# Kernel tuning notes

Hardware: AMD Instinct MI355X
Metric: run time of the kernel (lower is better)

## Reference

```python
import jax, jax.numpy as jnp
import numpy as np
import math

N = 100000      # nodes
E = 1600000     # edges
D = 128         # in_channels
C = 256         # number of dominant-set cliques
HID = 64        # mlp_hidden
RATIO = 0.8
K = int(math.ceil(RATIO * N))  # 80000 topk nodes per view


def setup_inputs() -> dict:
    key = jax.random.key(0)
    ks = jax.random.split(key, 18)
    s = 0.05
    return {
        "x": jax.random.normal(ks[0], (N, D), jnp.float32),
        "edge_index": jax.random.randint(ks[1], (2, E), 0, N, dtype=jnp.int32),
        "batch": jnp.zeros((N,), jnp.int32),
        "cluster_id": jax.random.randint(ks[2], (N,), 0, C, dtype=jnp.int32),
        # MLP scorer: Linear(D,HID) -> ReLU -> Linear(HID,1)
        "mlp_w1": jax.random.normal(ks[3], (D, HID), jnp.float32) * s,
        "mlp_b1": jnp.zeros((HID,), jnp.float32),
        "mlp_w2": jax.random.normal(ks[4], (HID, 1), jnp.float32) * s,
        "mlp_b2": jnp.zeros((1,), jnp.float32),
        # GATConv(D, 1, heads=1)
        "gat_w": jax.random.normal(ks[5], (D, 1), jnp.float32) * s,
        "gat_a_src": jax.random.normal(ks[6], (1,), jnp.float32) * s,
        "gat_a_dst": jax.random.normal(ks[7], (1,), jnp.float32) * s,
        "gat_b": jnp.zeros((1,), jnp.float32),
        # InterChannelGCN attention Linear(2D,1) split into fine/coarse halves
        "att_w_fine": jax.random.normal(ks[8], (D,), jnp.float32) * s,
        "att_w_coarse": jax.random.normal(ks[9], (D,), jnp.float32) * s,
        "att_b": jnp.zeros((1,), jnp.float32),
        # InterChannelGCN transform Linear(D,D)
        "trans_w": jax.random.normal(ks[10], (D, D), jnp.float32) * s,
        "trans_b": jnp.zeros((D,), jnp.float32),
    }


def _inter_channel_gcn(h_fine, H_coarse, R, wa, wb, ab, tw, tb):
    # attention(Linear(2D,1)) on concat(h_fine_i, H_coarse_j) == h_fine@wa + H_coarse@wb + b
    scores = h_fine @ wa[:, None] + (H_coarse @ wb)[None, :] + ab[0]   # [K, C]
    attn = jax.nn.softmax(scores * R, axis=-1)                          # mask-by-multiply, as original
    out = attn @ H_coarse + h_fine                                      # add_self=True
    return jax.nn.relu(out @ tw + tb)                                   # normalize=False


def reference(x, edge_index, batch, cluster_id,
              mlp_w1, mlp_b1, mlp_w2, mlp_b2,
              gat_w, gat_a_src, gat_a_dst, gat_b,
              att_w_fine, att_w_coarse, att_b, trans_w, trans_b):
    src, dst = edge_index[0], edge_index[1]

    # --- DominantClustering('avg'): cluster means as coarse features ---
    counts = jax.ops.segment_sum(jnp.ones((N,), jnp.float32), cluster_id, num_segments=C)
    Hcoarse = jax.ops.segment_sum(x, cluster_id, num_segments=C) / jnp.maximum(counts, 1.0)[:, None]

    # --- feature view: MLP score + topk ---
    feature_score = (jax.nn.relu(x @ mlp_w1 + mlp_b1) @ mlp_w2 + mlp_b2)[:, 0]   # [N]
    _, feat_idx = jax.lax.top_k(feature_score, K)
    feature_view3 = x[feat_idx]
    R_feat = jax.nn.one_hot(cluster_id[feat_idx], C, dtype=x.dtype)              # relationship matrix
    fuse1 = _inter_channel_gcn(feature_view3, Hcoarse, R_feat,
                               att_w_fine, att_w_coarse, att_b, trans_w, trans_b)

    # --- local view: GATConv(D,1,heads=1) score + topk ---
    h = x @ gat_w                                                                 # [N,1]
    e = jax.nn.leaky_relu(gat_a_src[0] * h[src, 0] + gat_a_dst[0] * h[dst, 0], 0.2)  # [E]
    m = jax.ops.segment_max(e, dst, num_segments=N)
    ex = jnp.exp(e - m[dst])
    den = jax.ops.segment_sum(ex, dst, num_segments=N)
    alpha = ex / jnp.maximum(den[dst], 1e-16)
    localview_score = jax.ops.segment_sum(alpha * h[src, 0], dst, num_segments=N) + gat_b[0]
    _, local_idx = jax.lax.top_k(localview_score, K)
    local_view1 = x[local_idx]
    R_local = jax.nn.one_hot(cluster_id[local_idx], C, dtype=x.dtype)
    fuse2 = _inter_channel_gcn(local_view1, Hcoarse, R_local,
                               att_w_fine, att_w_coarse, att_b, trans_w, trans_b)

    # --- union, edge filtering + remapping (padded fixed shapes) ---
    in_feat = jnp.zeros((N,), bool).at[feat_idx].set(True)
    in_local = jnp.zeros((N,), bool).at[local_idx].set(True)
    union = in_feat | in_local
    mapping = jnp.where(union, jnp.cumsum(union.astype(jnp.int32)) - 1, -1)
    m0, m1 = mapping[src], mapping[dst]
    valid = (m0 >= 0) & (m1 >= 0)
    edge_index_topk = jnp.where(valid[None, :], jnp.stack([m0, m1]), -1)          # [2,E], -1 = dropped

    # --- fused features (faithful to original's fuse1/fuse2 index swap) ---
    A = jnp.zeros((N, D), x.dtype).at[feat_idx].set(fuse2)    # fuse2 indexed by feature topk position
    B = jnp.zeros((N, D), x.dtype).at[local_idx].set(fuse1)   # fuse1 indexed by local topk position
    both = in_feat & in_local
    Fp = jnp.where(both[:, None], (A + B) * 0.5, A + B)
    Fp = jnp.where(union[:, None], Fp, 0.0)                   # [N,D], zero outside union

    new_batch = jnp.where(union, batch, -1)
    return Fp, edge_index_topk, new_batch
```

## Files before the change

### kernel.cpp

```cpp
#include <hip/hip_runtime.h>
#include <hip/hip_bf16.h>
#include <stdint.h>

#define N 100000
#define E_ 1600000
#define D 128
#define C_ 256
#define HID 64
#define KSEL 80000
#define NB 4096
#define CHUNK 1024
#define NCHUNK ((N + CHUNK - 1) / CHUNK)
#define CSEG 32
#define NBK 782
#define BCAP 2560
#define RMAX 2048

typedef __attribute__((ext_vector_type(8))) short bf16x8;
typedef __attribute__((ext_vector_type(4))) float f32x4;

__device__ __forceinline__ unsigned enc_f(float f) {
  unsigned b = __float_as_uint(f);
  return (b & 0x80000000u) ? ~b : (b | 0x80000000u);
}
__device__ __forceinline__ float dec_f(unsigned u) {
  unsigned b = (u & 0x80000000u) ? (u ^ 0x80000000u) : ~u;
  return __uint_as_float(b);
}

__device__ __forceinline__ unsigned short f2bf(float f) {
  unsigned u = __float_as_uint(f);
  unsigned r = u + 0x7FFFu + ((u >> 16) & 1u);
  return (unsigned short)(r >> 16);
}

__global__ __launch_bounds__(256) void k_hist_cluster(const int* __restrict__ cid, int* __restrict__ ccount) {
  int n = blockIdx.x * 256 + threadIdx.x;
  if (n < N) atomicAdd(&ccount[cid[n]], 1);
}

__global__ __launch_bounds__(1024) void k_scan_small(const int* __restrict__ in0, int* __restrict__ out0, int n) {
  __shared__ int sums[1024];
  const int* in = in0 + (size_t)blockIdx.x * n;
  int* out = out0 + (size_t)blockIdx.x * n;
  int t = threadIdx.x;
  int per = (n + 1023) / 1024;
  int base = t * per;
  int loc = 0;
  for (int k = 0; k < per; ++k) { int i = base + k; if (i < n) loc += in[i]; }
  sums[t] = loc; __syncthreads();
  for (int off = 1; off < 1024; off <<= 1) {
    int v = (t >= off) ? sums[t - off] : 0;
    __syncthreads();
    sums[t] += v;
    __syncthreads();
  }
  int run = (t == 0) ? 0 : sums[t - 1];
  for (int k = 0; k < per; ++k) { int i = base + k; if (i < n) { out[i] = run; run += in[i]; } }
}

__global__ __launch_bounds__(256) void k_scatter_cluster(const int* __restrict__ cid, const int* __restrict__ cstart,
                                                         int* __restrict__ ccur, int* __restrict__ cslot) {
  int n = blockIdx.x * 256 + threadIdx.x;
  if (n < N) {
    int c = cid[n];
    int p = cstart[c] + atomicAdd(&ccur[c], 1);
    cslot[p] = n;
  }
}

__global__ __launch_bounds__(128) void k_cluster_partial(const float* __restrict__ x, const int* __restrict__ cstart,
                                                         const int* __restrict__ ccount, const int* __restrict__ cslot,
                                                         float* __restrict__ Hc) {
  int c = blockIdx.x >> 5;
  int s = blockIdx.x & (CSEG - 1);
  int d = threadIdx.x;
  int st = cstart[c], cnt = ccount[c];
  int seg = (cnt + CSEG - 1) / CSEG;
  int lo = s * seg;
  int hi = min(cnt, lo + seg);
  if (lo >= hi) return;
  float acc = 0.f;
  int k = lo;
  for (; k + 2 <= hi; k += 2) {
    int n0 = cslot[st + k], n1 = cslot[st + k + 1];
    float v0 = x[(size_t)n0 * D + d];
    float v1 = x[(size_t)n1 * D + d];
    acc += v0 + v1;
  }
  if (k < hi) acc += x[(size_t)cslot[st + k] * D + d];
  atomicAdd(&Hc[(size_t)c * D + d], acc);
}

__global__ __launch_bounds__(128) void k_mean_gdot(const int* __restrict__ ccount, const float* __restrict__ wb,
                                                   float* __restrict__ Hc, float* __restrict__ gdot) {
  __shared__ float red[128];
  int c = blockIdx.x, d = threadIdx.x;
  float hv = Hc[(size_t)c * D + d] / (float)max(ccount[c], 1);
  Hc[(size_t)c * D + d] = hv;
  red[d] = hv * wb[d];
  __syncthreads();
  if (d < 64) {
    float v = red[d] + red[d + 64];
    for (int off = 32; off; off >>= 1) v += __shfl_down(v, off);
    if (d == 0) gdot[c] = v;
  }
}

__global__ __launch_bounds__(128) void k_S_SW_HW(const float* __restrict__ Hc, const float* __restrict__ tw,
                                                 float* __restrict__ SW, float* __restrict__ HW) {
  __shared__ float Sl[128];
  int b = blockIdx.x, t = threadIdx.x;
  if (b == 0) {
    float s = 0.f;
    for (int c = 0; c < C_; ++c) s += Hc[(size_t)c * D + t];
    Sl[t] = s;
    __syncthreads();
    float acc = 0.f;
    for (int d = 0; d < D; ++d) acc = fmaf(Sl[d], tw[(size_t)d * D + t], acc);
    SW[t] = acc;
  } else {
    const float* src = Hc + (size_t)(b - 1) * D;
    float acc = 0.f;
    for (int d = 0; d < D; ++d) acc = fmaf(src[d], tw[(size_t)d * D + t], acc);
    HW[(size_t)(b - 1) * D + t] = acc;
  }
}

__global__ __launch_bounds__(128) void k_twT(const float* __restrict__ tw, unsigned short* __restrict__ twT) {
  int k = blockIdx.x;
  int o = threadIdx.x;
  twT[(size_t)o * D + k] = f2bf(tw[(size_t)k * D + o]);
}

__global__ __launch_bounds__(256, 4) void k_score64(const float* __restrict__ x, const float* __restrict__ w1,
                                                    const float* __restrict__ b1, const float* __restrict__ w2,
                                                    const float* __restrict__ b2, const float* __restrict__ gw,
                                                    const float* __restrict__ wa, float* __restrict__ scoreF,
                                                    float* __restrict__ hg, float* __restrict__ aDot,
                                                    unsigned* __restrict__ mm) {
  __shared__ float xld[64 * D];
  __shared__ unsigned bmm[2];
  int tid = threadIdx.x;
  int base = blockIdx.x * 64;
  if (tid == 0) { bmm[0] = 0u; bmm[1] = 0xFFFFFFFFu; }
#pragma unroll
  for (int k = 0; k < 8; ++k) {
    int i = k * 256 + tid;
    int r = i >> 5, cc = i & 31;
    int n = base + r;
    float4 v = make_float4(0.f, 0.f, 0.f, 0.f);
    if (n < N) v = ((const float4*)(x + (size_t)n * D))[cc];
    ((float4*)xld)[r * 32 + (cc ^ (r & 7))] = v;
  }
  __syncthreads();

  int rg = tid >> 4;
  int cg = tid & 15;
  int r0 = rg * 4;
  int c4 = cg * 4;
  float acc[4][4] = {};
  float4 wc0 = *(const float4*)(w1 + (size_t)0 * HID + c4);
  float4 wc1 = *(const float4*)(w1 + (size_t)1 * HID + c4);
  float4 wc2 = *(const float4*)(w1 + (size_t)2 * HID + c4);
  float4 wc3 = *(const float4*)(w1 + (size_t)3 * HID + c4);
  float4 xc[4];
#pragma unroll
  for (int rr = 0; rr < 4; ++rr) {
    int row = r0 + rr;
    xc[rr] = ((const float4*)xld)[row * 32 + (row & 7)];
  }
  for (int d4 = 0; d4 < D; d4 += 4) {
    float4 wn0, wn1, wn2, wn3, xn[4];
    if (d4 + 4 < D) {
      wn0 = *(const float4*)(w1 + (size_t)(d4 + 4) * HID + c4);
      wn1 = *(const float4*)(w1 + (size_t)(d4 + 5) * HID + c4);
      wn2 = *(const float4*)(w1 + (size_t)(d4 + 6) * HID + c4);
      wn3 = *(const float4*)(w1 + (size_t)(d4 + 7) * HID + c4);
      int jn = (d4 >> 2) + 1;
#pragma unroll
      for (int rr = 0; rr < 4; ++rr) {
        int row = r0 + rr;
        xn[rr] = ((const float4*)xld)[row * 32 + (jn ^ (row & 7))];
      }
    } else {
      wn0 = wn1 = wn2 = wn3 = make_float4(0.f, 0.f, 0.f, 0.f);
#pragma unroll
      for (int rr = 0; rr < 4; ++rr) xn[rr] = make_float4(0.f, 0.f, 0.f, 0.f);
    }
#pragma unroll
    for (int rr = 0; rr < 4; ++rr) {
      float4 xv = xc[rr];
      acc[rr][0] = fmaf(xv.x, wc0.x, acc[rr][0]);
      acc[rr][1] = fmaf(xv.x, wc0.y, acc[rr][1]);
      acc[rr][2] = fmaf(xv.x, wc0.z, acc[rr][2]);
      acc[rr][3] = fmaf(xv.x, wc0.w, acc[rr][3]);
      acc[rr][0] = fmaf(xv.y, wc1.x, acc[rr][0]);
      acc[rr][1] = fmaf(xv.y, wc1.y, acc[rr][1]);
      acc[rr][2] = fmaf(xv.y, wc1.z, acc[rr][2]);
      acc[rr][3] = fmaf(xv.y, wc1.w, acc[rr][3]);
      acc[rr][0] = fmaf(xv.z, wc2.x, acc[rr][0]);
      acc[rr][1] = fmaf(xv.z, wc2.y, acc[rr][1]);
      acc[rr][2] = fmaf(xv.z, wc2.z, acc[rr][2]);
      acc[rr][3] = fmaf(xv.z, wc2.w, acc[rr][3]);
      acc[rr][0] = fmaf(xv.w, wc3.x, acc[rr][0]);
      acc[rr][1] = fmaf(xv.w, wc3.y, acc[rr][1]);
      acc[rr][2] = fmaf(xv.w, wc3.z, acc[rr][2]);
      acc[rr][3] = fmaf(xv.w, wc3.w, acc[rr][3]);
    }
    wc0 = wn0; wc1 = wn1; wc2 = wn2; wc3 = wn3;
#pragma unroll
    for (int rr = 0; rr < 4; ++rr) xc[rr] = xn[rr];
  }

  float4 b1v = *(const float4*)(b1 + c4);
  float4 w2v = *(const float4*)(w2 + c4);
  float bb = b2[0];
  unsigned vmx = 0u, vmn = 0xFFFFFFFFu;
#pragma unroll
  for (int rr = 0; rr < 4; ++rr) {
    float p = fmaxf(acc[rr][0] + b1v.x, 0.f) * w2v.x
            + fmaxf(acc[rr][1] + b1v.y, 0.f) * w2v.y
            + fmaxf(acc[rr][2] + b1v.z, 0.f) * w2v.z
            + fmaxf(acc[rr][3] + b1v.w, 0.f) * w2v.w;
#pragma unroll
    for (int off = 8; off; off >>= 1) p += __shfl_xor(p, off);
    if (cg == 0) {
      int n = base + r0 + rr;
      if (n < N) {
        float sf = p + bb;
        scoreF[n] = sf;
        unsigned e = enc_f(sf);
        vmx = max(vmx, e);
        vmn = min(vmn, e);
      }
    }
  }
#pragma unroll
  for (int off = 32; off; off >>= 1) {
    vmx = max(vmx, (unsigned)__shfl_xor((int)vmx, off));
    vmn = min(vmn, (unsigned)__shfl_xor((int)vmn, off));
  }
  if ((tid & 63) == 0) { atomicMax(&bmm[0], vmx); atomicMin(&bmm[1], vmn); }

  float4 gwa = *(const float4*)(gw + c4);
  float4 gwb = *(const float4*)(gw + 64 + c4);
  float4 waa = *(const float4*)(wa + c4);
  float4 wab = *(const float4*)(wa + 64 + c4);
#pragma unroll
  for (int rr = 0; rr < 4; ++rr) {
    int row = r0 + rr;
    float4 xa = ((const float4*)xld)[row * 32 + (cg ^ (row & 7))];
    float4 xb = ((const float4*)xld)[row * 32 + ((cg + 16) ^ (row & 7))];
    float hp = xa.x * gwa.x + xa.y * gwa.y + xa.z * gwa.z + xa.w * gwa.w
             + xb.x * gwb.x + xb.y * gwb.y + xb.z * gwb.z + xb.w * gwb.w;
    float ap = xa.x * waa.x + xa.y * waa.y + xa.z * waa.z + xa.w * waa.w
             + xb.x * wab.x + xb.y * wab.y + xb.z * wab.z + xb.w * wab.w;
#pragma unroll
    for (int off = 8; off; off >>= 1) {
      hp += __shfl_xor(hp, off);
      ap += __shfl_xor(ap, off);
    }
    if (cg == 0) {
      int n = base + row;
      if (n < N) { hg[n] = hp; aDot[n] = ap; }
    }
  }
  __syncthreads();
  if (tid == 0) { atomicMax(&mm[0], bmm[0]); atomicMin(&mm[2], bmm[1]); }
}

__global__ __launch_bounds__(1024) void k_escatter(const int* __restrict__ ei, const float* __restrict__ hg,
                                                   const float* __restrict__ asrc, const float* __restrict__ adst,
                                                   int* __restrict__ gcnt, uint2* __restrict__ payload) {
  __shared__ int lcnt[NBK];
  __shared__ int lbase[NBK];
  int tid = threadIdx.x;
  for (int i = tid; i < NBK; i += 1024) lcnt[i] = 0;
  int e0 = blockIdx.x * 8192;
  int es[8], ed[8];
#pragma unroll
  for (int k = 0; k < 8; ++k) {
    int e = e0 + k * 1024 + tid;
    bool v = (e < E_);
    es[k] = v ? ei[e] : -1;
    ed[k] = v ? ei[E_ + e] : -1;
  }
  __syncthreads();
#pragma unroll
  for (int k = 0; k < 8; ++k)
    if (ed[k] >= 0) atomicAdd(&lcnt[ed[k] >> 7], 1);
  __syncthreads();
  for (int i = tid; i < NBK; i += 1024) {
    int c = lcnt[i];
    lbase[i] = c ? atomicAdd(&gcnt[i], c) : 0;
    lcnt[i] = 0;
  }
  __syncthreads();
  float as = asrc[0], ad = adst[0];
#pragma unroll
  for (int k = 0; k < 8; ++k) {
    if (ed[k] < 0) continue;
    int s = es[k], d = ed[k];
    int b = d >> 7, dl = d & 127;
    float z = as * hg[s] + ad * hg[d];
    float ev = (z > 0.f) ? z : 0.2f * z;
    int pos = lbase[b] + atomicAdd(&lcnt[b], 1);
    if (pos < BCAP) {
      uint2 rec;
      rec.x = __float_as_uint(ev);
      rec.y = (unsigned)s | ((unsigned)dl << 24);
      payload[(size_t)b * BCAP + pos] = rec;
    }
  }
}

__global__ __launch_bounds__(256) void k_esoftmax(const uint2* __restrict__ payload, const int* __restrict__ gcnt,
                                                  const float* __restrict__ hg, const float* __restrict__ gb,
                                                  float* __restrict__ scoreL, unsigned* __restrict__ mm) {
  __shared__ unsigned mS[128];
  __shared__ float dS[128];
  __shared__ float nS[128];
  __shared__ unsigned bmm[2];
  int b = blockIdx.x;
  int tid = threadIdx.x;
  if (tid < 128) { mS[tid] = 0u; dS[tid] = 0.f; nS[tid] = 0.f; }
  if (tid == 0) { bmm[0] = 0u; bmm[1] = 0xFFFFFFFFu; }
  __syncthreads();
  int cnt = min(gcnt[b], BCAP);
  const uint2* bp = payload + (size_t)b * BCAP;
  for (int i = tid; i < cnt; i += 256) {
    uint2 r = bp[i];
    atomicMax(&mS[r.y >> 24], enc_f(__uint_as_float(r.x)));
  }
  __syncthreads();
  for (int i = tid; i < cnt; i += 256) {
    uint2 r = bp[i];
    int d = r.y >> 24;
    float ex = expf(__uint_as_float(r.x) - dec_f(mS[d]));
    float h = hg[r.y & 0xFFFFFFu];
    atomicAdd(&dS[d], ex);
    atomicAdd(&nS[d], ex * h);
  }
  __syncthreads();
  unsigned vmx = 0u, vmn = 0xFFFFFFFFu;
  if (tid < 128) {
    int dst = b * 128 + tid;
    if (dst < N) {
      float sl = nS[tid] / fmaxf(dS[tid], 1e-16f) + gb[0];
      scoreL[dst] = sl;
      unsigned e = enc_f(sl);
      vmx = e; vmn = e;
    }
  }
#pragma unroll
  for (int off = 32; off; off >>= 1) {
    vmx = max(vmx, (unsigned)__shfl_xor((int)vmx, off));
    vmn = min(vmn, (unsigned)__shfl_xor((int)vmn, off));
  }
  if ((tid & 63) == 0) { atomicMax(&bmm[0], vmx); atomicMin(&bmm[1], vmn); }
  __syncthreads();
  if (tid == 0) { atomicMax(&mm[1], bmm[0]); atomicMin(&mm[3], bmm[1]); }
}

__global__ __launch_bounds__(256) void k_bucket_hist2(const float* __restrict__ sc2, const unsigned* __restrict__ mm,
                                                      int* __restrict__ bucket2, int* __restrict__ hist2) {
  int v = blockIdx.y;
  int n = blockIdx.x * 256 + threadIdx.x;
  if (n >= N) return;
  const float* sc = sc2 + (size_t)v * N;
  float smax = dec_f(mm[v]), smin = dec_f(mm[2 + v]);
  float range = smax - smin;
  float scale = (range > 0.f) ? ((float)NB / range) : 0.f;
  float t = (smax - sc[n]) * scale;
  int b = (int)t;
  b = b < 0 ? 0 : (b > NB - 1 ? NB - 1 : b);
  bucket2[(size_t)v * N + n] = b;
  atomicAdd(&hist2[v * NB + b], 1);
}

__global__ __launch_bounds__(256) void k_bucket_scatter2(const int* __restrict__ bucket2, const int* __restrict__ start2,
                                                         int* __restrict__ cur2, int* __restrict__ slot2) {
  int v = blockIdx.y;
  int n = blockIdx.x * 256 + threadIdx.x;
  if (n >= N) return;
  int b = bucket2[(size_t)v * N + n];
  slot2[(size_t)v * N + start2[v * NB + b] + atomicAdd(&cur2[v * NB + b], 1)] = n;
}

__global__ __launch_bounds__(64) void k_bucket_rank3(const float* __restrict__ sc2, const int* __restrict__ start2,
                                                     const int* __restrict__ hist2, const int* __restrict__ slot2,
                                                     int* __restrict__ rank2, int* __restrict__ sorted2) {
  __shared__ unsigned long long keys[RMAX];
  int v = blockIdx.y;
  int b = blockIdx.x;
  int st = start2[v * NB + b], cnt = hist2[v * NB + b];
  if (cnt == 0) return;
  const float* sc = sc2 + (size_t)v * N;
  const int* slot = slot2 + (size_t)v * N;
  int* rank = rank2 + (size_t)v * N;
  int* sorted = sorted2 + (size_t)v * N;
  int tid = threadIdx.x;
  if (cnt <= RMAX) {
    for (int i = tid; i < cnt; i += 64) {
      int m = slot[st + i];
      keys[i] = (((unsigned long long)(~enc_f(sc[m]))) << 32) | (unsigned)m;
    }
    __syncthreads();
    for (int i = tid; i < cnt; i += 64) {
      unsigned long long mykey = keys[i];
      int r = 0;
      for (int j = 0; j < cnt; ++j) r += (keys[j] < mykey) ? 1 : 0;
      int m = (int)(mykey & 0xFFFFFFFFu);
      rank[m] = st + r;
      sorted[st + r] = m;
    }
  } else {
    for (int i = tid; i < cnt; i += 64) {
      int m = slot[st + i];
      unsigned long long mykey = (((unsigned long long)(~enc_f(sc[m]))) << 32) | (unsigned)m;
      int r = 0;
      for (int j = 0; j < cnt; ++j) {
        int mj = slot[st + j];
        unsigned long long k = (((unsigned long long)(~enc_f(sc[mj]))) << 32) | (unsigned)mj;
        r += (k < mykey) ? 1 : 0;
      }
      rank[m] = st + r;
      sorted[st + r] = m;
    }
  }
}

__global__ __launch_bounds__(1024) void k_union_chunksum(const int* __restrict__ rankF, const int* __restrict__ rankL,
                                                         int* __restrict__ csum) {
  __shared__ int red[1024];
  int t = threadIdx.x; int i = blockIdx.x * 1024 + t;
  int u = (i < N) ? (((rankF[i] < KSEL) || (rankL[i] < KSEL)) ? 1 : 0) : 0;
  red[t] = u; __syncthreads();
  for (int off = 512; off; off >>= 1) { if (t < off) red[t] += red[t + off]; __syncthreads(); }
  if (t == 0) csum[blockIdx.x] = red[0];
}

__global__ __launch_bounds__(1024) void k_union_map(const int* __restrict__ rankF, const int* __restrict__ rankL,
                                                    const int* __restrict__ cstart, const int* __restrict__ batch,
                                                    int* __restrict__ mapping, float* __restrict__ outBatch) {
  __shared__ int sums[1024];
  int t = threadIdx.x; int i = blockIdx.x * 1024 + t;
  int u = (i < N) ? (((rankF[i] < KSEL) || (rankL[i] < KSEL)) ? 1 : 0) : 0;
  sums[t] = u; __syncthreads();
  for (int off = 1; off < 1024; off <<= 1) {
    int v = (t >= off) ? sums[t - off] : 0;
    __syncthreads();
    sums[t] += v;
    __syncthreads();
  }
  if (i < N) {
    mapping[i] = u ? (cstart[blockIdx.x] + sums[t] - 1) : -1;
    outBatch[i] = u ? (float)batch[i] : -1.0f;
  }
}

__global__ __launch_bounds__(256) void k_edge_out(const int* __restrict__ ei, const int* __restrict__ mapping,
                                                  float* __restrict__ outE) {
  int e = blockIdx.x * 256 + threadIdx.x;
  if (e >= E_) return;
  int m0 = mapping[ei[e]], m1 = mapping[ei[E_ + e]];
  bool valid = (m0 >= 0) && (m1 >= 0);
  outE[e] = valid ? (float)m0 : -1.f;
  outE[E_ + e] = valid ? (float)m1 : -1.f;
}

__global__ __launch_bounds__(256) void k_zero_rows(const int* __restrict__ mapping, float* __restrict__ Fp) {
  int i = blockIdx.x * 256 + threadIdx.x;
  int n = i >> 5;
  if (n < N && mapping[n] < 0) ((float4*)Fp)[i] = make_float4(0.f, 0.f, 0.f, 0.f);
}

__global__ __launch_bounds__(256, 4) void k_fuse64(const float* __restrict__ x, const unsigned short* __restrict__ twT,
                                                   const float* __restrict__ tb, const float* __restrict__ SW,
                                                   const float* __restrict__ HW, const float* __restrict__ gdot,
                                                   const float* __restrict__ aDot, const int* __restrict__ cid,
                                                   const int* __restrict__ srcL, const int* __restrict__ tgtL,
                                                   const float* __restrict__ attb, const int* __restrict__ rankF,
                                                   float* __restrict__ Fp, int accum) {
  __shared__ __align__(16) unsigned xw[64 * 64];
  __shared__ float pq[64 * 2];
  __shared__ int mt[64 * 2];
  __shared__ int ft[64];
  int tid = threadIdx.x;
  int base = blockIdx.x * 64;
  if (tid < 64) {
    int ws = srcL[base + tid];
    int cc = cid[ws];
    int tg = tgtL[base + tid];
    mt[tid * 2] = cc;
    mt[tid * 2 + 1] = tg;
    ft[tid] = (rankF[tg] < KSEL) ? 1 : 0;
    float s = aDot[ws] + gdot[cc] + attb[0];
    float mx = fmaxf(s, 0.f);
    float esm = expf(s - mx), eom = expf(-mx);
    float dn = esm + 255.f * eom;
    pq[tid * 2] = esm / dn;
    pq[tid * 2 + 1] = eom / dn;
  }
#pragma unroll
  for (int k = 0; k < 8; ++k) {
    int i = k * 256 + tid;
    int r = i >> 5, c4 = i & 31;
    int ws = srcL[base + r];
    float4 v = ((const float4*)(x + (size_t)ws * D))[c4];
    uint2 pk;
    pk.x = (unsigned)f2bf(v.x) | ((unsigned)f2bf(v.y) << 16);
    pk.y = (unsigned)f2bf(v.z) | ((unsigned)f2bf(v.w) << 16);
    int u2 = r * 32 + (c4 ^ ((r & 7) << 1));
    ((uint2*)xw)[u2] = pk;
  }
  __syncthreads();

  int w = tid >> 6;
  int l = tid & 63;
  int nl = l & 15;
  int khalf = l >> 4;
  int row = w * 16 + nl;

  f32x4 acc[8] = {};
  const char* xbase = (const char*)xw + row * 256;
  unsigned rsw = (unsigned)((row & 7) << 4);
  bf16x8 bfr[4];
#pragma unroll
  for (int ks = 0; ks < 4; ++ks)
    bfr[ks] = *(const bf16x8*)(xbase + (((unsigned)(ks * 64 + khalf * 16)) ^ rsw));
#pragma unroll
  for (int ks = 0; ks < 4; ++ks) {
#pragma unroll
    for (int ot = 0; ot < 8; ++ot) {
      bf16x8 afrag = *(const bf16x8*)(twT + (size_t)(ot * 16 + nl) * D + ks * 32 + khalf * 8);
      acc[ot] = __builtin_amdgcn_mfma_f32_16x16x32_bf16(afrag, bfr[ks], acc[ot], 0, 0, 0);
    }
  }

  float p = pq[row * 2], q = pq[row * 2 + 1];
  int cc = mt[row * 2];
  int tgt = mt[row * 2 + 1];
  int doAcc = accum && ft[row];
#pragma unroll
  for (int ot = 0; ot < 8; ++ot) {
    int ch = ot * 16 + khalf * 4;
    float4 tbv = *(const float4*)(tb + ch);
    float4 swv = *(const float4*)(SW + ch);
    float4 hw = *(const float4*)(HW + (size_t)cc * D + ch);
    float4 o;
    o.x = fmaxf(acc[ot][0] + tbv.x + q * swv.x + (p - q) * hw.x, 0.f);
    o.y = fmaxf(acc[ot][1] + tbv.y + q * swv.y + (p - q) * hw.y, 0.f);
    o.z = fmaxf(acc[ot][2] + tbv.z + q * swv.z + (p - q) * hw.z, 0.f);
    o.w = fmaxf(acc[ot][3] + tbv.w + q * swv.w + (p - q) * hw.w, 0.f);
    float4* dst = (float4*)(Fp + (size_t)tgt * D + ch);
    if (doAcc) {
      float4 old = *dst;
      o.x = (o.x + old.x) * 0.5f;
      o.y = (o.y + old.y) * 0.5f;
      o.z = (o.z + old.z) * 0.5f;
      o.w = (o.w + old.w) * 0.5f;
    }
    *dst = o;
  }
}

extern "C" void kernel_launch(void* const* d_in, const int* in_sizes, int n_in,
                              void* d_out, int out_size, void* d_ws, size_t ws_size,
                              hipStream_t stream) {
  const float* x   = (const float*)d_in[0];
  const int* ei    = (const int*)d_in[1];
  const int* batch = (const int*)d_in[2];
  const int* cid   = (const int*)d_in[3];
  const float* w1  = (const float*)d_in[4];
  const float* b1  = (const float*)d_in[5];
  const float* w2  = (const float*)d_in[6];
  const float* b2  = (const float*)d_in[7];
  const float* gw  = (const float*)d_in[8];
  const float* gas = (const float*)d_in[9];
  const float* gad = (const float*)d_in[10];
  const float* gb  = (const float*)d_in[11];
  const float* wa  = (const float*)d_in[12];
  const float* wb  = (const float*)d_in[13];
  const float* ab  = (const float*)d_in[14];
  const float* tw  = (const float*)d_in[15];
  const float* tb  = (const float*)d_in[16];
  (void)in_sizes; (void)n_in; (void)ws_size; (void)out_size;

  char* p = (char*)d_ws;
  auto alloc = [&](size_t bytes) -> char* {
    char* r = p;
    p += (bytes + 255) & ~(size_t)255;
    return r;
  };
  int* ccount    = (int*)alloc(C_ * 4);
  int* ccur      = (int*)alloc(C_ * 4);
  unsigned* mm   = (unsigned*)alloc(16);
  int* hist2     = (int*)alloc(2 * NB * 4);
  int* cur2      = (int*)alloc(2 * NB * 4);
  float* Hc      = (float*)alloc((size_t)C_ * D * 4);
  int* gcnt      = (int*)alloc(NBK * 4);
  size_t zeroBytes = (size_t)(p - (char*)d_ws);
  int* cstart   = (int*)alloc(C_ * 4);
  int* cslot    = (int*)alloc((size_t)N * 4);
  float* gdot   = (float*)alloc(C_ * 4);
  float* SW     = (float*)alloc(D * 4);
  float* HW     = (float*)alloc((size_t)C_ * D * 4);
  unsigned short* twT = (unsigned short*)alloc((size_t)D * D * 2);
  float* score2 = (float*)alloc((size_t)2 * N * 4);
  float* hg     = (float*)alloc((size_t)N * 4);
  float* aDot   = (float*)alloc((size_t)N * 4);
  uint2* payload = (uint2*)alloc((size_t)NBK * BCAP * 8);
  int* bucket2  = (int*)alloc((size_t)2 * N * 4);
  int* start2   = (int*)alloc(2 * NB * 4);
  int* slot2    = (int*)alloc((size_t)2 * N * 4);
  int* sorted2  = (int*)alloc((size_t)2 * N * 4);
  int* rank2    = (int*)alloc((size_t)2 * N * 4);
  int* csums    = (int*)alloc(NCHUNK * 4);
  int* cstarts  = (int*)alloc(NCHUNK * 4);
  int* mapping  = (int*)alloc((size_t)N * 4);

  float* scoreF = score2;
  float* scoreL = score2 + N;
  int* sortedF  = sorted2;
  int* sortedL  = sorted2 + N;
  int* rankF    = rank2;
  int* rankL    = rank2 + N;

  float* outF = (float*)d_out;
  float* outE = outF + (size_t)N * D;
  float* outB = outE + (size_t)2 * E_;

  hipMemsetAsync(d_ws, 0, zeroBytes, stream);
  hipMemsetAsync(mm + 2, 0xFF, 8, stream);

  k_hist_cluster<<<(N + 255) / 256, 256, 0, stream>>>(cid, ccount);
  k_scan_small<<<1, 1024, 0, stream>>>(ccount, cstart, C_);
  k_scatter_cluster<<<(N + 255) / 256, 256, 0, stream>>>(cid, cstart, ccur, cslot);
  k_cluster_partial<<<C_ * CSEG, 128, 0, stream>>>(x, cstart, ccount, cslot, Hc);
  k_mean_gdot<<<C_, 128, 0, stream>>>(ccount, wb, Hc, gdot);
  k_S_SW_HW<<<C_ + 1, 128, 0, stream>>>(Hc, tw, SW, HW);
  k_twT<<<D, D, 0, stream>>>(tw, twT);

  k_score64<<<(N + 63) / 64, 256, 0, stream>>>(x, w1, b1, w2, b2, gw, wa, scoreF, hg, aDot, mm);
  k_escatter<<<(E_ + 8191) / 8192, 1024, 0, stream>>>(ei, hg, gas, gad, gcnt, payload);
  k_esoftmax<<<NBK, 256, 0, stream>>>(payload, gcnt, hg, gb, scoreL, mm);

  dim3 g2((N + 255) / 256, 2);
  k_bucket_hist2<<<g2, 256, 0, stream>>>(score2, mm, bucket2, hist2);
  k_scan_small<<<2, 1024, 0, stream>>>(hist2, start2, NB);
  k_bucket_scatter2<<<g2, 256, 0, stream>>>(bucket2, start2, cur2, slot2);
  dim3 gr(NB, 2);
  k_bucket_rank3<<<gr, 64, 0, stream>>>(score2, start2, hist2, slot2, rank2, sorted2);

  k_union_chunksum<<<NCHUNK, 1024, 0, stream>>>(rankF, rankL, csums);
  k_scan_small<<<1, 1024, 0, stream>>>(csums, cstarts, NCHUNK);
  k_union_map<<<NCHUNK, 1024, 0, stream>>>(rankF, rankL, cstarts, batch, mapping, outB);
  k_edge_out<<<(E_ + 255) / 256, 256, 0, stream>>>(ei, mapping, outE);
  k_zero_rows<<<(N * 32 + 255) / 256, 256, 0, stream>>>(mapping, outF);

  k_fuse64<<<KSEL / 64, 256, 0, stream>>>(x, twT, tb, SW, HW, gdot, aDot, cid, sortedL, sortedF, ab, rankF, outF, 0);
  k_fuse64<<<KSEL / 64, 256, 0, stream>>>(x, twT, tb, SW, HW, gdot, aDot, cid, sortedF, sortedL, ab, rankF, outF, 1);
}
```

Measured before the change: 566.4 us.

## Shrink edge payload to 4 bytes and recompute attention logits in softmax

The edge scatter kernel no longer computes the GAT logit or gathers hg. It writes only a packed source and local-destination word, which halves payload memory traffic. The softmax kernel caches per-bucket destination hg in shared memory and recomputes the leaky-relu logit in both passes from a gathered hg[src]. Separately, the score kernel drops the register prefetch of x tiles from LDS and the block-level min/max reduction, issuing global atomics per wavefront instead. This trades extra random hg gathers and more global atomics for less payload bandwidth and lower register pressure.

```diff
diff --git a/kernel.cpp b/kernel.cpp
--- a/kernel.cpp
+++ b/kernel.cpp
@@ -140,10 +140,8 @@
                                                     float* __restrict__ hg, float* __restrict__ aDot,
                                                     unsigned* __restrict__ mm) {
   __shared__ float xld[64 * D];
-  __shared__ unsigned bmm[2];
   int tid = threadIdx.x;
   int base = blockIdx.x * 64;
-  if (tid == 0) { bmm[0] = 0u; bmm[1] = 0xFFFFFFFFu; }
 #pragma unroll
   for (int k = 0; k < 8; ++k) {
     int i = k * 256 + tid;
@@ -164,33 +162,21 @@
   float4 wc1 = *(const float4*)(w1 + (size_t)1 * HID + c4);
   float4 wc2 = *(const float4*)(w1 + (size_t)2 * HID + c4);
   float4 wc3 = *(const float4*)(w1 + (size_t)3 * HID + c4);
-  float4 xc[4];
-#pragma unroll
-  for (int rr = 0; rr < 4; ++rr) {
-    int row = r0 + rr;
-    xc[rr] = ((const float4*)xld)[row * 32 + (row & 7)];
-  }
   for (int d4 = 0; d4 < D; d4 += 4) {
-    float4 wn0, wn1, wn2, wn3, xn[4];
+    float4 wn0, wn1, wn2, wn3;
     if (d4 + 4 < D) {
       wn0 = *(const float4*)(w1 + (size_t)(d4 + 4) * HID + c4);
       wn1 = *(const float4*)(w1 + (size_t)(d4 + 5) * HID + c4);
       wn2 = *(const float4*)(w1 + (size_t)(d4 + 6) * HID + c4);
       wn3 = *(const float4*)(w1 + (size_t)(d4 + 7) * HID + c4);
-      int jn = (d4 >> 2) + 1;
-#pragma unroll
-      for (int rr = 0; rr < 4; ++rr) {
-        int row = r0 + rr;
-        xn[rr] = ((const float4*)xld)[row * 32 + (jn ^ (row & 7))];
-      }
     } else {
       wn0 = wn1 = wn2 = wn3 = make_float4(0.f, 0.f, 0.f, 0.f);
-#pragma unroll
-      for (int rr = 0; rr < 4; ++rr) xn[rr] = make_float4(0.f, 0.f, 0.f, 0.f);
-    }
+    }
+    int j = d4 >> 2;
 #pragma unroll
     for (int rr = 0; rr < 4; ++rr) {
-      float4 xv = xc[rr];
+      int row = r0 + rr;
+      float4 xv = ((const float4*)xld)[row * 32 + (j ^ (row & 7))];
       acc[rr][0] = fmaf(xv.x, wc0.x, acc[rr][0]);
       acc[rr][1] = fmaf(xv.x, wc0.y, acc[rr][1]);
       acc[rr][2] = fmaf(xv.x, wc0.z, acc[rr][2]);
@@ -209,8 +195,6 @@
       acc[rr][3] = fmaf(xv.w, wc3.w, acc[rr][3]);
     }
     wc0 = wn0; wc1 = wn1; wc2 = wn2; wc3 = wn3;
-#pragma unroll
-    for (int rr = 0; rr < 4; ++rr) xc[rr] = xn[rr];
   }
 
   float4 b1v = *(const float4*)(b1 + c4);
@@ -241,7 +225,7 @@
     vmx = max(vmx, (unsigned)__shfl_xor((int)vmx, off));
     vmn = min(vmn, (unsigned)__shfl_xor((int)vmn, off));
   }
-  if ((tid & 63) == 0) { atomicMax(&bmm[0], vmx); atomicMin(&bmm[1], vmn); }
+  if ((tid & 63) == 0) { atomicMax(&mm[0], vmx); atomicMin(&mm[2], vmn); }
 
   float4 gwa = *(const float4*)(gw + c4);
   float4 gwb = *(const float4*)(gw + 64 + c4);
@@ -266,13 +250,10 @@
       if (n < N) { hg[n] = hp; aDot[n] = ap; }
     }
   }
-  __syncthreads();
-  if (tid == 0) { atomicMax(&mm[0], bmm[0]); atomicMin(&mm[2], bmm[1]); }
-}
-
-__global__ __launch_bounds__(1024) void k_escatter(const int* __restrict__ ei, const float* __restrict__ hg,
-                                                   const float* __restrict__ asrc, const float* __restrict__ adst,
-                                                   int* __restrict__ gcnt, uint2* __restrict__ payload) {
+}
+
+__global__ __launch_bounds__(1024) void k_escatter(const int* __restrict__ ei, int* __restrict__ gcnt,
+                                                   unsigned* __restrict__ payload) {
   __shared__ int lcnt[NBK];
   __shared__ int lbase[NBK];
   int tid = threadIdx.x;
@@ -297,50 +278,54 @@
     lcnt[i] = 0;
   }
   __syncthreads();
-  float as = asrc[0], ad = adst[0];
 #pragma unroll
   for (int k = 0; k < 8; ++k) {
     if (ed[k] < 0) continue;
     int s = es[k], d = ed[k];
     int b = d >> 7, dl = d & 127;
-    float z = as * hg[s] + ad * hg[d];
-    float ev = (z > 0.f) ? z : 0.2f * z;
     int pos = lbase[b] + atomicAdd(&lcnt[b], 1);
-    if (pos < BCAP) {
-      uint2 rec;
-      rec.x = __float_as_uint(ev);
-      rec.y = (unsigned)s | ((unsigned)dl << 24);
-      payload[(size_t)b * BCAP + pos] = rec;
-    }
-  }
-}
-
-__global__ __launch_bounds__(256) void k_esoftmax(const uint2* __restrict__ payload, const int* __restrict__ gcnt,
-                                                  const float* __restrict__ hg, const float* __restrict__ gb,
+    if (pos < BCAP) payload[(size_t)b * BCAP + pos] = (unsigned)s | ((unsigned)dl << 24);
+  }
+}
+
+__global__ __launch_bounds__(256) void k_esoftmax(const unsigned* __restrict__ payload, const int* __restrict__ gcnt,
+                                                  const float* __restrict__ hg, const float* __restrict__ asrc,
+                                                  const float* __restrict__ adst, const float* __restrict__ gb,
                                                   float* __restrict__ scoreL, unsigned* __restrict__ mm) {
   __shared__ unsigned mS[128];
   __shared__ float dS[128];
   __shared__ float nS[128];
+  __shared__ float hgl[128];
   __shared__ unsigned bmm[2];
   int b = blockIdx.x;
   int tid = threadIdx.x;
-  if (tid < 128) { mS[tid] = 0u; dS[tid] = 0.f; nS[tid] = 0.f; }
+  if (tid < 128) {
+    mS[tid] = 0u; dS[tid] = 0.f; nS[tid] = 0.f;
+    int g = b * 128 + tid;
+    hgl[tid] = (g < N) ? hg[g] : 0.f;
+  }
   if (tid == 0) { bmm[0] = 0u; bmm[1] = 0xFFFFFFFFu; }
   __syncthreads();
+  float as = asrc[0], ad = adst[0];
   int cnt = min(gcnt[b], BCAP);
-  const uint2* bp = payload + (size_t)b * BCAP;
+  const unsigned* bp = payload + (size_t)b * BCAP;
   for (int i = tid; i < cnt; i += 256) {
-    uint2 r = bp[i];
-    atomicMax(&mS[r.y >> 24], enc_f(__uint_as_float(r.x)));
+    unsigned r = bp[i];
+    int s = (int)(r & 0xFFFFFFu), dl = (int)(r >> 24);
+    float z = as * hg[s] + ad * hgl[dl];
+    float ev = (z > 0.f) ? z : 0.2f * z;
+    atomicMax(&mS[dl], enc_f(ev));
   }
   __syncthreads();
   for (int i = tid; i < cnt; i += 256) {
-    uint2 r = bp[i];
-    int d = r.y >> 24;
-    float ex = expf(__uint_as_float(r.x) - dec_f(mS[d]));
-    float h = hg[r.y & 0xFFFFFFu];
-    atomicAdd(&dS[d], ex);
-    atomicAdd(&nS[d], ex * h);
+    unsigned r = bp[i];
+    int s = (int)(r & 0xFFFFFFu), dl = (int)(r >> 24);
+    float h = hg[s];
+    float z = as * h + ad * hgl[dl];
+    float ev = (z > 0.f) ? z : 0.2f * z;
+    float ex = expf(ev - dec_f(mS[dl]));
+    atomicAdd(&dS[dl], ex);
+    atomicAdd(&nS[dl], ex * h);
   }
   __syncthreads();
   unsigned vmx = 0u, vmn = 0xFFFFFFFFu;
@@ -611,7 +596,7 @@
   float* score2 = (float*)alloc((size_t)2 * N * 4);
   float* hg     = (float*)alloc((size_t)N * 4);
   float* aDot   = (float*)alloc((size_t)N * 4);
-  uint2* payload = (uint2*)alloc((size_t)NBK * BCAP * 8);
+  unsigned* payload = (unsigned*)alloc((size_t)NBK * BCAP * 4);
   int* bucket2  = (int*)alloc((size_t)2 * N * 4);
   int* start2   = (int*)alloc(2 * NB * 4);
   int* slot2    = (int*)alloc((size_t)2 * N * 4);
@@ -644,8 +629,8 @@
   k_twT<<<D, D, 0, stream>>>(tw, twT);
 
   k_score64<<<(N + 63) / 64, 256, 0, stream>>>(x, w1, b1, w2, b2, gw, wa, scoreF, hg, aDot, mm);
-  k_escatter<<<(E_ + 8191) / 8192, 1024, 0, stream>>>(ei, hg, gas, gad, gcnt, payload);
-  k_esoftmax<<<NBK, 256, 0, stream>>>(payload, gcnt, hg, gb, scoreL, mm);
+  k_escatter<<<(E_ + 8191) / 8192, 1024, 0, stream>>>(ei, gcnt, payload);
+  k_esoftmax<<<NBK, 256, 0, stream>>>(payload, gcnt, hg, gas, gad, gb, scoreL, mm);
 
   dim3 g2((N + 255) / 256, 2);
   k_bucket_hist2<<<g2, 256, 0, stream>>>(score2, mm, bucket2, hist2);
```

Measured after the change: 669.8 us. 1.18x slower.
